# Kernel optimization log

Measured on AMD Instinct MI355X. Metric: run time of the kernel, lower is better.

The kernel has to match this reference:

```python
import math
import jax, jax.numpy as jnp
import numpy as np

B, S, D, H = 4, 2048, 1024, 16
HD = D // H
EPS = 1e-5
NEG = 1e10


def setup_inputs() -> dict:
    key = jax.random.key(0)
    ks = jax.random.split(key, 6)
    std = 0.02
    return {
        "x": jax.random.normal(ks[0], (B, S, D), dtype=jnp.float32),
        "ln1_w": jnp.ones((D,), jnp.float32),
        "ln1_b": jnp.zeros((D,), jnp.float32),
        "W_attn": jax.random.normal(ks[1], (D, 3 * D), jnp.float32) * std,
        "b_attn": jnp.zeros((3 * D,), jnp.float32),
        "W_cproj": jax.random.normal(ks[2], (D, D), jnp.float32) * std,
        "b_cproj": jnp.zeros((D,), jnp.float32),
        "ln2_w": jnp.ones((D,), jnp.float32),
        "ln2_b": jnp.zeros((D,), jnp.float32),
        "W_fc": jax.random.normal(ks[3], (D, 4 * D), jnp.float32) * std,
        "b_fc": jnp.zeros((4 * D,), jnp.float32),
        "W_mproj": jax.random.normal(ks[4], (4 * D, D), jnp.float32) * std,
        "b_mproj": jnp.zeros((D,), jnp.float32),
    }


def _layernorm(x, w, b):
    u = jnp.mean(x, axis=-1, keepdims=True)
    s = jnp.mean((x - u) ** 2, axis=-1, keepdims=True)
    return w * ((x - u) / jnp.sqrt(s + EPS)) + b


def _gelu(x):
    return 0.5 * x * (1 + jnp.tanh(math.sqrt(2 / math.pi) * (x + 0.044715 * x ** 3)))


def _block(x, ln1_w, ln1_b, W_attn, b_attn, W_cproj, b_cproj,
           ln2_w, ln2_b, W_fc, b_fc, W_mproj, b_mproj):
    h = _layernorm(x, ln1_w, ln1_b)
    qkv = h @ W_attn + b_attn                       # [B,S,3D]
    q, k, v = jnp.split(qkv, 3, axis=-1)
    # split heads -> [B,H,S,hd]
    q = q.reshape(B, S, H, HD).transpose(0, 2, 1, 3)
    k = k.reshape(B, S, H, HD).transpose(0, 2, 1, 3)
    v = v.reshape(B, S, H, HD).transpose(0, 2, 1, 3)
    w = jnp.einsum('bhqd,bhkd->bhqk', q, k) / math.sqrt(HD)
    bias = jnp.tril(jnp.ones((S, S), jnp.float32))  # causal mask
    w = w * bias - NEG * (1 - bias)
    w = jax.nn.softmax(w, axis=-1)
    a = jnp.einsum('bhqk,bhkd->bhqd', w, v)
    a = a.transpose(0, 2, 1, 3).reshape(B, S, D)    # merge heads
    a = a @ W_cproj + b_cproj
    x = x + a                                        # residual
    m = _layernorm(x, ln2_w, ln2_b)
    m = _gelu(m @ W_fc + b_fc) @ W_mproj + b_mproj
    return x + m


def reference(x, ln1_w, ln1_b, W_attn, b_attn, W_cproj, b_cproj,
              ln2_w, ln2_b, W_fc, b_fc, W_mproj, b_mproj):
    return _block(x, ln1_w, ln1_b, W_attn, b_attn, W_cproj, b_cproj,
                  ln2_w, ln2_b, W_fc, b_fc, W_mproj, b_mproj)
```

## Files before the change

kernel.cpp:

```cpp
#include <hip/hip_runtime.h>
#include <hip/hip_bf16.h>
#include <math.h>


typedef __attribute__((ext_vector_type(8))) short short8;
typedef __attribute__((ext_vector_type(4))) float floatx4;
typedef __attribute__((ext_vector_type(2))) unsigned int uint2v;

#define MFMA16(a, b, c) __builtin_amdgcn_mfma_f32_16x16x32_bf16((a), (b), (c), 0, 0, 0)

__device__ __forceinline__ short f2bf(float f) {
    union { float f; unsigned u; } a; a.f = f;
    unsigned r = a.u + 0x7fffu + ((a.u >> 16) & 1u);
    return (short)(r >> 16);
}

__device__ __forceinline__ float bf2f(unsigned short u) {
    union { unsigned u; float f; } a; a.u = ((unsigned)u) << 16;
    return a.f;
}

__device__ __forceinline__ float fast_rcp(float x) {
#if defined(__HIP_DEVICE_COMPILE__)
    return __builtin_amdgcn_rcpf(x);
#else
    return 1.0f / x;
#endif
}

__device__ __forceinline__ float gelu_f(float x) {
    const float u = x + 0.044715f * x * x * x;
    const float t = exp2f(2.302118131f * u);
    return x - x * fast_rcp(t + 1.0f);
}

__device__ __forceinline__ void gload_lds16(const short* g, short* l) {
    __builtin_amdgcn_global_load_lds((const __attribute__((address_space(1))) void*)g,
                                     (__attribute__((address_space(3))) void*)l, 16, 0, 0);
}

__global__ void tcast_kernel(const float* __restrict__ W, short* __restrict__ Wt,
                             int K, int N) {
    __shared__ float tile[32][33];
    const int bx = blockIdx.x * 32;
    const int by = blockIdx.y * 32;
    const int tx = threadIdx.x;
    const int ty = threadIdx.y;
#pragma unroll
    for (int i = 0; i < 32; i += 8)
        tile[ty + i][tx] = W[(size_t)(by + ty + i) * N + bx + tx];
    __syncthreads();
#pragma unroll
    for (int i = 0; i < 32; i += 8)
        Wt[(size_t)(bx + ty + i) * K + by + tx] = f2bf(tile[tx][ty + i]);
}

__global__ __launch_bounds__(256) void ln_kernel(const float* __restrict__ x,
                                                 const float* __restrict__ w,
                                                 const float* __restrict__ b,
                                                 short* __restrict__ out) {
    const int row = blockIdx.x;
    const int t = threadIdx.x;
    const float4 v = ((const float4*)(x + (size_t)row * 1024))[t];
    float s = v.x + v.y + v.z + v.w;
    float s2 = v.x * v.x + v.y * v.y + v.z * v.z + v.w * v.w;
#pragma unroll
    for (int d = 32; d >= 1; d >>= 1) {
        s += __shfl_xor(s, d, 64);
        s2 += __shfl_xor(s2, d, 64);
    }
    __shared__ float red[8];
    const int wid = t >> 6, lane = t & 63;
    if (lane == 0) { red[wid * 2] = s; red[wid * 2 + 1] = s2; }
    __syncthreads();
    s = red[0] + red[2] + red[4] + red[6];
    s2 = red[1] + red[3] + red[5] + red[7];
    const float mean = s * (1.f / 1024.f);
    const float var = s2 * (1.f / 1024.f) - mean * mean;
    const float rstd = rsqrtf(var + 1e-5f);
    const float4 wv = ((const float4*)w)[t];
    const float4 bv = ((const float4*)b)[t];
    union { ushort4 u; short sa[4]; } ov;
    ov.sa[0] = f2bf(wv.x * ((v.x - mean) * rstd) + bv.x);
    ov.sa[1] = f2bf(wv.y * ((v.y - mean) * rstd) + bv.y);
    ov.sa[2] = f2bf(wv.z * ((v.z - mean) * rstd) + bv.z);
    ov.sa[3] = f2bf(wv.w * ((v.w - mean) * rstd) + bv.w);
    ((ushort4*)(out + (size_t)row * 1024))[t] = ov.u;
}

__global__ __launch_bounds__(256) void reduce_kernel(
    const unsigned short* __restrict__ p0, const unsigned short* __restrict__ p1,
    const float* __restrict__ bias, const float* __restrict__ res,
    float* __restrict__ out) {
    const int row = blockIdx.x;
    const int t = threadIdx.x;
    const size_t off = (size_t)row * 1024;
    const ushort4 a = ((const ushort4*)(p0 + off))[t];
    const ushort4 c = ((const ushort4*)(p1 + off))[t];
    const float4 r = ((const float4*)(res + off))[t];
    const float4 bv = ((const float4*)bias)[t];
    float4 o;
    o.x = bf2f(a.x) + bf2f(c.x) + bv.x + r.x;
    o.y = bf2f(a.y) + bf2f(c.y) + bv.y + r.y;
    o.z = bf2f(a.z) + bf2f(c.z) + bv.z + r.z;
    o.w = bf2f(a.w) + bf2f(c.w) + bv.w + r.w;
    ((float4*)(out + off))[t] = o;
}

__global__ __launch_bounds__(256) void reduce_ln_kernel(
    const unsigned short* __restrict__ p0, const unsigned short* __restrict__ p1,
    const float* __restrict__ bias, const float* __restrict__ res,
    float* __restrict__ x2out,
    const float* __restrict__ w, const float* __restrict__ b,
    short* __restrict__ hout) {
    const int row = blockIdx.x;
    const int t = threadIdx.x;
    const size_t off = (size_t)row * 1024;
    const ushort4 a = ((const ushort4*)(p0 + off))[t];
    const ushort4 c = ((const ushort4*)(p1 + off))[t];
    const float4 r = ((const float4*)(res + off))[t];
    const float4 bv = ((const float4*)bias)[t];
    float4 v;
    v.x = bf2f(a.x) + bf2f(c.x) + bv.x + r.x;
    v.y = bf2f(a.y) + bf2f(c.y) + bv.y + r.y;
    v.z = bf2f(a.z) + bf2f(c.z) + bv.z + r.z;
    v.w = bf2f(a.w) + bf2f(c.w) + bv.w + r.w;
    ((float4*)(x2out + off))[t] = v;
    float s = v.x + v.y + v.z + v.w;
    float s2 = v.x * v.x + v.y * v.y + v.z * v.z + v.w * v.w;
#pragma unroll
    for (int d = 32; d >= 1; d >>= 1) {
        s += __shfl_xor(s, d, 64);
        s2 += __shfl_xor(s2, d, 64);
    }
    __shared__ float red[8];
    const int wid = t >> 6, lane = t & 63;
    if (lane == 0) { red[wid * 2] = s; red[wid * 2 + 1] = s2; }
    __syncthreads();
    s = red[0] + red[2] + red[4] + red[6];
    s2 = red[1] + red[3] + red[5] + red[7];
    const float mean = s * (1.f / 1024.f);
    const float var = s2 * (1.f / 1024.f) - mean * mean;
    const float rstd = rsqrtf(var + 1e-5f);
    const float4 wv = ((const float4*)w)[t];
    const float4 lb = ((const float4*)b)[t];
    union { ushort4 u; short sa[4]; } ov;
    ov.sa[0] = f2bf(wv.x * ((v.x - mean) * rstd) + lb.x);
    ov.sa[1] = f2bf(wv.y * ((v.y - mean) * rstd) + lb.y);
    ov.sa[2] = f2bf(wv.z * ((v.z - mean) * rstd) + lb.z);
    ov.sa[3] = f2bf(wv.w * ((v.w - mean) * rstd) + lb.w);
    ((ushort4*)(hout + (size_t)row * 1024))[t] = ov.u;
}

template <int EPI>
__global__ __launch_bounds__(256) void gemm_kernel(
    const short* __restrict__ A, const short* __restrict__ Bt,
    const float* __restrict__ bias,
    void* __restrict__ Cout, int M, int N, int Klen, int lda, int ldb) {
    __shared__ __align__(16) short As[128][32];
    __shared__ __align__(16) short Bs[128][32];

    const int tid = threadIdx.x;
    const int wid = tid >> 6;
    const int lane = tid & 63;
    const int quad = lane >> 4;
    const int l16 = lane & 15;
    const int wm = (wid >> 1) * 64;
    const int wn = (wid & 1) * 64;

    const unsigned gx = gridDim.x;
    const unsigned bid2 = blockIdx.x + gx * blockIdx.y;
    const unsigned xcd = bid2 & 7;
    const unsigned loc = bid2 >> 3;
    const unsigned nb = loc % gx;
    const unsigned mhi = loc / gx;
    const int m0 = (int)(mhi * 8 + xcd) * 128;
    const int n0 = (int)nb * 128;
    const int kbase = blockIdx.z * Klen;

    const int lr = lane >> 2;
    const int lc = (lane & 3) * 8;

    floatx4 acc[4][4] = {};

    const short* ga0 = A + (size_t)(m0 + wid * 16 + lr) * lda + kbase + lc;
    const short* ga1 = A + (size_t)(m0 + 64 + wid * 16 + lr) * lda + kbase + lc;
    const short* gb0 = Bt + (size_t)(n0 + wid * 16 + lr) * ldb + kbase + lc;
    const short* gb1 = Bt + (size_t)(n0 + 64 + wid * 16 + lr) * ldb + kbase + lc;
    short* lA0 = &As[wid * 16][0];
    short* lA1 = &As[64 + wid * 16][0];
    short* lB0 = &Bs[wid * 16][0];
    short* lB1 = &Bs[64 + wid * 16][0];

    for (int k0 = 0; k0 < Klen; k0 += 32) {
        gload_lds16(ga0 + k0, lA0);
        gload_lds16(ga1 + k0, lA1);
        gload_lds16(gb0 + k0, lB0);
        gload_lds16(gb1 + k0, lB1);
        __syncthreads();
        short8 af[4], bf[4];
#pragma unroll
        for (int mt = 0; mt < 4; mt++)
            af[mt] = *(const short8*)&As[wm + mt * 16 + l16][quad * 8];
#pragma unroll
        for (int nt = 0; nt < 4; nt++)
            bf[nt] = *(const short8*)&Bs[wn + nt * 16 + l16][quad * 8];
#pragma unroll
        for (int mt = 0; mt < 4; mt++)
#pragma unroll
            for (int nt = 0; nt < 4; nt++)
                acc[mt][nt] = MFMA16(af[mt], bf[nt], acc[mt][nt]);
        __syncthreads();
    }
#pragma unroll
    for (int nt = 0; nt < 4; nt++) {
        const int col = n0 + wn + nt * 16 + l16;
        const float bv = (EPI == 3) ? 0.f : bias[col];
#pragma unroll
        for (int mt = 0; mt < 4; mt++) {
#pragma unroll
            for (int r = 0; r < 4; r++) {
                const int row = m0 + wm + mt * 16 + quad * 4 + r;
                const size_t idx = (size_t)row * N + col;
                float v = acc[mt][nt][r] + bv;
                if constexpr (EPI == 0) {
                    ((short*)Cout)[idx] = f2bf(v);
                } else if constexpr (EPI == 1) {
                    ((short*)Cout)[idx] = f2bf(gelu_f(v));
                } else {
                    ((short*)Cout)[(size_t)blockIdx.z * M * N + idx] = f2bf(v);
                }
            }
        }
    }
}

#define GBAR()  asm volatile("s_barrier" ::: "memory")
#define LGKM0() asm volatile("s_waitcnt lgkmcnt(0)" ::: "memory")
#define STAGE_A(b_, kt_, p_)                                                   \
    do {                                                                       \
        gload_lds16(gA + (size_t)((p_) * 128) * lda + (kt_) * 64,              \
                    lA + (b_) * 16384 + (p_) * 8192);                          \
        gload_lds16(gA + (size_t)((p_) * 128 + 64) * lda + (kt_) * 64,         \
                    lA + (b_) * 16384 + (p_) * 8192 + 4096);                   \
    } while (0)
#define STAGE_B(b_, kt_, p_)                                                   \
    do {                                                                       \
        gload_lds16(gB + (size_t)((p_) * 128) * ldb + (kt_) * 64,              \
                    lB + (b_) * 16384 + (p_) * 8192);                          \
        gload_lds16(gB + (size_t)((p_) * 128 + 64) * ldb + (kt_) * 64,         \
                    lB + (b_) * 16384 + (p_) * 8192 + 4096);                   \
    } while (0)

template <int EPI>
__global__ __launch_bounds__(512, 2) void gemm256_kernel(
    const short* __restrict__ A, const short* __restrict__ Bt,
    const float* __restrict__ bias,
    void* __restrict__ Cout, int M, int N, int Klen, int lda, int ldb) {
    extern __shared__ __align__(16) short lds[];
    short* As = lds;
    short* Bs = lds + 32768;

    const int tid = threadIdx.x;
    const int wid = tid >> 6;
    const int lane = tid & 63;
    const int quad = lane >> 4;
    const int l16 = lane & 15;
    const int l7 = l16 & 7;
    const int warp_m = wid >> 2;
    const int warp_n = wid & 3;

    const unsigned gx = gridDim.x;
    const unsigned bid2 = blockIdx.x + gx * blockIdx.y;
    const unsigned xcd = bid2 & 7;
    const unsigned loc = bid2 >> 3;
    const unsigned nb = loc % gx;
    const unsigned mhi = loc / gx;
    const int m0 = (int)(mhi * 8 + xcd) * 256;
    const int n0 = (int)nb * 256;
    const int kbase = blockIdx.z * Klen;
    const int NT = Klen >> 6;

    const int rsub = tid >> 3;
    const int scol = ((tid & 7) ^ (rsub & 7)) << 3;
    const short* gA = A + (size_t)(m0 + rsub) * lda + kbase + scol;
    const short* gB = Bt + (size_t)(n0 + rsub) * ldb + kbase + scol;
    short* lA = As + wid * 512;
    short* lB = Bs + wid * 512;

    const int sk0 = ((0 | quad) ^ l7) << 3;
    const int sk1 = ((4 | quad) ^ l7) << 3;

    floatx4 acc[8][4] = {};
    short8 afrag[4][2], bA[2][2], bB[2][2];

    STAGE_A(0, 0, 0); STAGE_A(0, 0, 1);
    STAGE_B(0, 0, 0); STAGE_B(0, 0, 1);
    if (NT > 1) {
        STAGE_A(1, 1, 0);
        asm volatile("s_waitcnt vmcnt(2)" ::: "memory");
    } else {
        asm volatile("s_waitcnt vmcnt(0)" ::: "memory");
    }
    GBAR();

    for (int t = 0; t < NT; ++t) {
        const int b = t & 1;
        const int bn = b ^ 1;
        const short* Ab = As + b * 16384 + (warp_m * 128 + l16) * 64;
        const short* Bb = Bs + b * 16384 + (warp_n * 64 + l16) * 64;
#pragma unroll
        for (int mi = 0; mi < 4; mi++) {
            afrag[mi][0] = *(const short8*)(Ab + mi * 1024 + sk0);
            afrag[mi][1] = *(const short8*)(Ab + mi * 1024 + sk1);
        }
#pragma unroll
        for (int ni = 0; ni < 2; ni++) {
            bA[ni][0] = *(const short8*)(Bb + ni * 1024 + sk0);
            bA[ni][1] = *(const short8*)(Bb + ni * 1024 + sk1);
        }
        if (t + 1 < NT) STAGE_A(bn, t + 1, 1);
        GBAR(); LGKM0();
        __builtin_amdgcn_s_setprio(1);
#pragma unroll
        for (int mi = 0; mi < 4; mi++)
#pragma unroll
            for (int ni = 0; ni < 2; ni++) {
                acc[mi][ni] = MFMA16(afrag[mi][0], bA[ni][0], acc[mi][ni]);
                acc[mi][ni] = MFMA16(afrag[mi][1], bA[ni][1], acc[mi][ni]);
            }
        __builtin_amdgcn_s_setprio(0);
        GBAR();
#pragma unroll
        for (int ni = 0; ni < 2; ni++) {
            bB[ni][0] = *(const short8*)(Bb + (2 + ni) * 1024 + sk0);
            bB[ni][1] = *(const short8*)(Bb + (2 + ni) * 1024 + sk1);
        }
        if (t + 1 < NT) STAGE_B(bn, t + 1, 0);
        GBAR(); LGKM0();
        __builtin_amdgcn_s_setprio(1);
#pragma unroll
        for (int mi = 0; mi < 4; mi++)
#pragma unroll
            for (int ni = 0; ni < 2; ni++) {
                acc[mi][2 + ni] = MFMA16(afrag[mi][0], bB[ni][0], acc[mi][2 + ni]);
                acc[mi][2 + ni] = MFMA16(afrag[mi][1], bB[ni][1], acc[mi][2 + ni]);
            }
        __builtin_amdgcn_s_setprio(0);
        GBAR();
#pragma unroll
        for (int mi = 0; mi < 4; mi++) {
            afrag[mi][0] = *(const short8*)(Ab + (4 + mi) * 1024 + sk0);
            afrag[mi][1] = *(const short8*)(Ab + (4 + mi) * 1024 + sk1);
        }
        if (t + 1 < NT) STAGE_B(bn, t + 1, 1);
        GBAR(); LGKM0();
        __builtin_amdgcn_s_setprio(1);
#pragma unroll
        for (int mi = 0; mi < 4; mi++)
#pragma unroll
            for (int ni = 0; ni < 2; ni++) {
                acc[4 + mi][2 + ni] = MFMA16(afrag[mi][0], bB[ni][0], acc[4 + mi][2 + ni]);
                acc[4 + mi][2 + ni] = MFMA16(afrag[mi][1], bB[ni][1], acc[4 + mi][2 + ni]);
            }
        __builtin_amdgcn_s_setprio(0);
        GBAR();
        if (t + 2 < NT) STAGE_A(b, t + 2, 0);
        GBAR();
        __builtin_amdgcn_s_setprio(1);
#pragma unroll
        for (int mi = 0; mi < 4; mi++)
#pragma unroll
            for (int ni = 0; ni < 2; ni++) {
                acc[4 + mi][ni] = MFMA16(afrag[mi][0], bA[ni][0], acc[4 + mi][ni]);
                acc[4 + mi][ni] = MFMA16(afrag[mi][1], bA[ni][1], acc[4 + mi][ni]);
            }
        __builtin_amdgcn_s_setprio(0);
        if (t + 2 < NT) asm volatile("s_waitcnt vmcnt(2)" ::: "memory");
        else            asm volatile("s_waitcnt vmcnt(0)" ::: "memory");
        GBAR();
    }

#pragma unroll
    for (int ni = 0; ni < 4; ni++) {
        const int col = n0 + warp_n * 64 + ni * 16 + l16;
        const float bv = (EPI == 3) ? 0.f : bias[col];
#pragma unroll
        for (int mi = 0; mi < 8; mi++) {
#pragma unroll
            for (int r = 0; r < 4; r++) {
                const int row = m0 + warp_m * 128 + mi * 16 + quad * 4 + r;
                const size_t idx = (size_t)row * N + col;
                float v = acc[mi][ni][r] + bv;
                if constexpr (EPI == 0) {
                    ((short*)Cout)[idx] = f2bf(v);
                } else if constexpr (EPI == 1) {
                    ((short*)Cout)[idx] = f2bf(gelu_f(v));
                } else {
                    ((short*)Cout)[(size_t)blockIdx.z * M * N + idx] = f2bf(v);
                }
            }
        }
    }
}
#undef STAGE_A
#undef STAGE_B
#undef GBAR
#undef LGKM0

__global__ __launch_bounds__(256) void attn_kernel(
    const short* __restrict__ qkv, short* __restrict__ aout,
    short* __restrict__ O0buf, float* __restrict__ m0p, float* __restrict__ l0p,
    float* __restrict__ m1p, float* __restrict__ l1p) {
    __shared__ __align__(16) short smem[9216];
    short* Ks = smem;
    short* Vt = smem + 64 * 72;

    const int tid = threadIdx.x;
    const int wid = tid >> 6;
    const int lane = tid & 63;
    const int quad = lane >> 4;
    const int l16 = lane & 15;

    const int y = blockIdx.y;
    int qt, ktlo, kthi, mode;
    if (y < 8)       { qt = 8 + y;        ktlo = 0;  kthi = 16;             mode = 1; }
    else if (y < 16) { qt = 15 - y;       ktlo = 0;  kthi = (qt + 1) * 2;   mode = 0; }
    else             { qt = 8 + (23 - y); ktlo = 16; kthi = (qt + 1) * 2;   mode = 2; }
    const int q0 = qt * 128;
    const int bh = blockIdx.x;
    const int b = bh >> 4;
    const int h = bh & 15;

    const short* base = qkv + (size_t)b * 2048 * 3072 + h * 64;
    const int qrow_base = q0 + wid * 32;

    short8 qf[2][2];
#pragma unroll
    for (int qt_i = 0; qt_i < 2; qt_i++)
#pragma unroll
        for (int ks = 0; ks < 2; ks++)
            qf[qt_i][ks] = *(const short8*)(base +
                (size_t)(qrow_base + qt_i * 16 + l16) * 3072 + ks * 32 + quad * 8);

    const unsigned vaddr =
        (unsigned)(size_t)(__attribute__((address_space(3))) void*)Vt +
        (unsigned)(quad * 128 + l16 * 8);

    union VF { short8 s; uint2v h2[2]; };
    union PK { short8 s; unsigned u[4]; };

    floatx4 o[4][2] = {};
    float mrow[2] = {-1e30f, -1e30f};
    float lrow[2] = {0.f, 0.f};
    const float SCL = 0.125f * 1.44269504f;

    for (int kt = ktlo; kt < kthi; kt++) {
        const int kt0 = kt * 64;
        {
            const int r = tid >> 2;
            const int dgi = tid & 3;
            const short* krow = base + (size_t)(kt0 + r) * 3072 + 1024 + dgi * 16;
            const short* vrow = base + (size_t)(kt0 + r) * 3072 + 2048 + dgi * 16;
            *(uint4*)&Ks[r * 72 + dgi * 16] = ((const uint4*)krow)[0];
            *(uint4*)&Ks[r * 72 + dgi * 16 + 8] = ((const uint4*)krow)[1];
            short* vdst = Vt + dgi * 1024 + (r >> 2) * 64 + (r & 3) * 16;
            *(uint4*)&vdst[0] = ((const uint4*)vrow)[0];
            *(uint4*)&vdst[8] = ((const uint4*)vrow)[1];
        }
        __syncthreads();
        if (kt0 <= qrow_base + 31) {
            floatx4 st[4][2] = {};
#pragma unroll
            for (int kti = 0; kti < 4; kti++) {
                const short8 kf0 = *(const short8*)&Ks[(kti * 16 + l16) * 72 + quad * 8];
                const short8 kf1 = *(const short8*)&Ks[(kti * 16 + l16) * 72 + 32 + quad * 8];
#pragma unroll
                for (int qt_i = 0; qt_i < 2; qt_i++) {
                    st[kti][qt_i] = MFMA16(kf0, qf[qt_i][0], st[kti][qt_i]);
                    st[kti][qt_i] = MFMA16(kf1, qf[qt_i][1], st[kti][qt_i]);
                }
            }
            VF vf[2][4];
#define TRRD(dst, offs) \
    asm volatile("ds_read_b64_tr_b16 %0, %1 offset:" offs : "=v"(dst) : "v"(vaddr))
            TRRD(vf[0][0].h2[0], "0");    TRRD(vf[0][0].h2[1], "512");
            TRRD(vf[0][1].h2[0], "2048"); TRRD(vf[0][1].h2[1], "2560");
            TRRD(vf[0][2].h2[0], "4096"); TRRD(vf[0][2].h2[1], "4608");
            TRRD(vf[0][3].h2[0], "6144"); TRRD(vf[0][3].h2[1], "6656");
            TRRD(vf[1][0].h2[0], "1024"); TRRD(vf[1][0].h2[1], "1536");
            TRRD(vf[1][1].h2[0], "3072"); TRRD(vf[1][1].h2[1], "3584");
            TRRD(vf[1][2].h2[0], "5120"); TRRD(vf[1][2].h2[1], "5632");
            TRRD(vf[1][3].h2[0], "7168"); TRRD(vf[1][3].h2[1], "7680");
#undef TRRD
            const bool needmask = (kt0 + 63) > qrow_base;
            PK pk[2][2];
#pragma unroll
            for (int qt_i = 0; qt_i < 2; qt_i++) {
                const int q = qrow_base + qt_i * 16 + l16;
                if (needmask) {
#pragma unroll
                    for (int kti = 0; kti < 4; kti++)
#pragma unroll
                        for (int r = 0; r < 4; r++)
                            if ((kt0 + kti * 16 + quad * 4 + r) > q) st[kti][qt_i][r] = -1e30f;
                }
                float mx = -1e30f;
#pragma unroll
                for (int kti = 0; kti < 4; kti++)
#pragma unroll
                    for (int r = 0; r < 4; r++) mx = fmaxf(mx, st[kti][qt_i][r]);
                mx = fmaxf(mx, __shfl_xor(mx, 16, 64));
                mx = fmaxf(mx, __shfl_xor(mx, 32, 64));
                const float mnew = fmaxf(mrow[qt_i], mx);
                const float alpha = exp2f((mrow[qt_i] - mnew) * SCL);
                mrow[qt_i] = mnew;
                const float nm = -mnew * SCL;
                float ps = 0.f;
#pragma unroll
                for (int kti = 0; kti < 4; kti++)
#pragma unroll
                    for (int r = 0; r < 4; r++) {
                        const float p = exp2f(fmaf(st[kti][qt_i][r], SCL, nm));
                        st[kti][qt_i][r] = p;
                        ps += p;
                    }
                ps += __shfl_xor(ps, 16, 64);
                ps += __shfl_xor(ps, 32, 64);
                lrow[qt_i] = lrow[qt_i] * alpha + ps;
#pragma unroll
                for (int dt = 0; dt < 4; dt++) o[dt][qt_i] *= alpha;
#define CVTPK(dst, lo, hi) \
    asm("v_cvt_pk_bf16_f32 %0, %1, %2" : "=v"(dst) : "v"(lo), "v"(hi))
                CVTPK(pk[0][qt_i].u[0], st[0][qt_i][0], st[0][qt_i][1]);
                CVTPK(pk[0][qt_i].u[1], st[0][qt_i][2], st[0][qt_i][3]);
                CVTPK(pk[0][qt_i].u[2], st[1][qt_i][0], st[1][qt_i][1]);
                CVTPK(pk[0][qt_i].u[3], st[1][qt_i][2], st[1][qt_i][3]);
                CVTPK(pk[1][qt_i].u[0], st[2][qt_i][0], st[2][qt_i][1]);
                CVTPK(pk[1][qt_i].u[1], st[2][qt_i][2], st[2][qt_i][3]);
                CVTPK(pk[1][qt_i].u[2], st[3][qt_i][0], st[3][qt_i][1]);
                CVTPK(pk[1][qt_i].u[3], st[3][qt_i][2], st[3][qt_i][3]);
#undef CVTPK
            }
            asm volatile("s_waitcnt lgkmcnt(0)" ::: "memory");
            __builtin_amdgcn_sched_barrier(0);
#pragma unroll
            for (int c = 0; c < 2; c++)
#pragma unroll
                for (int dt = 0; dt < 4; dt++) {
                    o[dt][0] = MFMA16(vf[c][dt].s, pk[c][0].s, o[dt][0]);
                    o[dt][1] = MFMA16(vf[c][dt].s, pk[c][1].s, o[dt][1]);
                }
        }
        __syncthreads();
    }
    const int slot = (qt - 8) * 64 + bh;
    short* Ow = smem + wid * (32 * 72);
    const float rl0 = (mode == 0) ? fast_rcp(lrow[0]) : 1.0f;
    const float rl1 = (mode == 0) ? fast_rcp(lrow[1]) : 1.0f;
#pragma unroll
    for (int dt = 0; dt < 4; dt++)
#pragma unroll
        for (int r = 0; r < 4; r++) {
            Ow[(l16) * 72 + dt * 16 + quad * 4 + r] = f2bf(o[dt][0][r] * rl0);
            Ow[(16 + l16) * 72 + dt * 16 + quad * 4 + r] = f2bf(o[dt][1][r] * rl1);
        }
    if (mode != 0 && quad == 0) {
        const int qi0 = slot * 128 + (qrow_base - q0) + l16;
        if (mode == 1) {
            m0p[qi0] = mrow[0]; l0p[qi0] = lrow[0];
            m0p[qi0 + 16] = mrow[1]; l0p[qi0 + 16] = lrow[1];
        } else {
            m1p[qi0] = mrow[0]; l1p[qi0] = lrow[0];
            m1p[qi0 + 16] = mrow[1]; l1p[qi0 + 16] = lrow[1];
        }
    }
    __asm__ volatile("s_waitcnt lgkmcnt(0)" ::: "memory");
    {
        const int ql = lane >> 1;
        const int h2 = lane & 1;
        short* orow;
        if (mode == 1)
            orow = O0buf + (size_t)slot * 8192 + (size_t)(wid * 32 + ql) * 64 + h2 * 32;
        else
            orow = aout + (size_t)(b * 2048 + q0 + wid * 32 + ql) * 1024 + h * 64 + h2 * 32;
#pragma unroll
        for (int s = 0; s < 4; s++)
            *(uint4*)(orow + s * 8) = *(const uint4*)&Ow[ql * 72 + h2 * 32 + s * 8];
    }
}

__global__ __launch_bounds__(256) void attn_combine_kernel(
    const short* __restrict__ O0buf, short* __restrict__ aout,
    const float* __restrict__ m0p, const float* __restrict__ l0p,
    const float* __restrict__ m1p, const float* __restrict__ l1p) {
    const int slot = blockIdx.x;
    const int qt = 8 + (slot >> 6);
    const int bh = slot & 63;
    const int b = bh >> 4;
    const int h = bh & 15;
    const int t = threadIdx.x;
    const float SCL = 0.125f * 1.44269504f;
#pragma unroll
    for (int rep = 0; rep < 2; rep++) {
        const int ql = rep * 64 + (t >> 2);
        const int dg = (t & 3) * 16;
        const int qi = slot * 128 + ql;
        const float m0 = m0p[qi], l0 = l0p[qi], m1 = m1p[qi], l1 = l1p[qi];
        const float mm = fmaxf(m0, m1);
        const float w0 = exp2f((m0 - mm) * SCL);
        const float w1 = exp2f((m1 - mm) * SCL);
        const float rl = fast_rcp(fmaf(l0, w0, l1 * w1));
        const float f0 = w0 * rl, f1 = w1 * rl;
        const short* p0 = O0buf + (size_t)slot * 8192 + (size_t)ql * 64 + dg;
        short* pout = aout + (size_t)(b * 2048 + qt * 128 + ql) * 1024 + h * 64 + dg;
        union { uint4 v; unsigned short u[8]; } a0, a1, ov;
#pragma unroll
        for (int half = 0; half < 2; half++) {
            a0.v = ((const uint4*)p0)[half];
            a1.v = ((const uint4*)pout)[half];
#pragma unroll
            for (int j = 0; j < 8; j++)
                ov.u[j] = (unsigned short)f2bf(bf2f(a0.u[j]) * f0 + bf2f(a1.u[j]) * f1);
            ((uint4*)pout)[half] = ov.v;
        }
    }
}

extern "C" void kernel_launch(void* const* d_in, const int* in_sizes, int n_in,
                              void* d_out, int out_size, void* d_ws, size_t ws_size,
                              hipStream_t stream) {
    const float* x       = (const float*)d_in[0];
    const float* ln1_w   = (const float*)d_in[1];
    const float* ln1_b   = (const float*)d_in[2];
    const float* W_attn  = (const float*)d_in[3];
    const float* b_attn  = (const float*)d_in[4];
    const float* W_cproj = (const float*)d_in[5];
    const float* b_cproj = (const float*)d_in[6];
    const float* ln2_w   = (const float*)d_in[7];
    const float* ln2_b   = (const float*)d_in[8];
    const float* W_fc    = (const float*)d_in[9];
    const float* b_fc    = (const float*)d_in[10];
    const float* W_mproj = (const float*)d_in[11];
    const float* b_mproj = (const float*)d_in[12];

    char* ws = (char*)d_ws;
    short* W1t  = (short*)(ws + 0);
    short* W2t  = (short*)(ws + 6291456);
    short* W3t  = (short*)(ws + 8388608);
    short* W4t  = (short*)(ws + 16777216);
    short* h    = (short*)(ws + 25165824);
    short* aout = (short*)(ws + 41943040);
    short* big  = (short*)(ws + 58720256);
    short* O0buf = h;
    float* m0p = (float*)(ws + 25165824 + 8388608);
    float* l0p = (float*)(ws + 25165824 + 8388608 + 262144);
    float* m1p = (float*)(ws + 25165824 + 8388608 + 524288);
    float* l1p = (float*)(ws + 25165824 + 8388608 + 786432);
    short* pbuf = h;
    float* x2   = (float*)d_out;
    float* out  = (float*)d_out;

    dim3 tb(32, 8);
    hipLaunchKernelGGL(tcast_kernel, dim3(96, 32), tb, 0, stream, W_attn, W1t, 1024, 3072);
    hipLaunchKernelGGL(tcast_kernel, dim3(32, 32), tb, 0, stream, W_cproj, W2t, 1024, 1024);
    hipLaunchKernelGGL(tcast_kernel, dim3(128, 32), tb, 0, stream, W_fc, W3t, 1024, 4096);
    hipLaunchKernelGGL(tcast_kernel, dim3(32, 128), tb, 0, stream, W_mproj, W4t, 4096, 1024);

    hipLaunchKernelGGL(ln_kernel, dim3(8192), dim3(256), 0, stream, x, ln1_w, ln1_b, h);

    hipLaunchKernelGGL((gemm256_kernel<0>), dim3(12, 32, 1), dim3(512), 131072, stream,
                       h, W1t, b_attn, (void*)big,
                       8192, 3072, 1024, 1024, 1024);

    hipLaunchKernelGGL(attn_kernel, dim3(64, 24), dim3(256), 0, stream,
                       big, aout, O0buf, m0p, l0p, m1p, l1p);
    hipLaunchKernelGGL(attn_combine_kernel, dim3(512), dim3(256), 0, stream,
                       O0buf, aout, m0p, l0p, m1p, l1p);

    hipLaunchKernelGGL((gemm_kernel<3>), dim3(8, 64, 2), dim3(256), 0, stream,
                       aout, W2t, (const float*)nullptr, (void*)big,
                       8192, 1024, 512, 1024, 1024);
    hipLaunchKernelGGL(reduce_ln_kernel, dim3(8192), dim3(256), 0, stream,
                       (const unsigned short*)big,
                       (const unsigned short*)(big + (size_t)8192 * 1024),
                       b_cproj, x, x2, ln2_w, ln2_b, h);

    hipLaunchKernelGGL((gemm256_kernel<1>), dim3(16, 32, 1), dim3(512), 131072, stream,
                       h, W3t, b_fc, (void*)big,
                       8192, 4096, 1024, 1024, 1024);

    hipLaunchKernelGGL((gemm256_kernel<3>), dim3(4, 32, 2), dim3(512), 131072, stream,
                       big, W4t, (const float*)nullptr, (void*)pbuf,
                       8192, 1024, 2048, 4096, 4096);
    hipLaunchKernelGGL(reduce_kernel, dim3(8192), dim3(256), 0, stream,
                       (const unsigned short*)pbuf,
                       (const unsigned short*)(pbuf + (size_t)8192 * 1024),
                       b_mproj, x2, out);
}
```

Baseline: 533.2 us.

## Register-prefetch next K/V tile in attention and use 256-tile GEMM for c_proj

The attention loop now loads the next K and V tile from global memory into registers while the current tile is being computed, then writes those registers to shared memory at the top of the next iteration. This hides global load latency behind the MFMA work. The V remap to the transposed layout is recomputed per lane so that each lane stores contiguous 16-byte chunks. Separately, the attention output projection switches from the 128-tile split-K GEMM to the 256-tile GEMM kernel. This changes the grid from 1024 to 256 blocks, which risks lower occupancy and a tail effect.

```diff
diff --git a/kernel.cpp b/kernel.cpp
--- a/kernel.cpp
+++ b/kernel.cpp
@@ -443,6 +443,14 @@
             qf[qt_i][ks] = *(const short8*)(base +
                 (size_t)(qrow_base + qt_i * 16 + l16) * 3072 + ks * 32 + quad * 8);
 
+    const int kr_ = tid >> 2;
+    const int kcg = (tid & 3) * 16;
+    const short* ksrc = base + 1024 + kcg;
+    short* kdst = &Ks[kr_ * 72 + kcg];
+    const int vrA = ((lane >> 3) << 2) | ((lane >> 1) & 3);
+    const short* vsrc = base + 2048 + wid * 16 + (lane & 1) * 8;
+    short* vdst = Vt + wid * 1024 + lane * 8;
+
     const unsigned vaddr =
         (unsigned)(size_t)(__attribute__((address_space(3))) void*)Vt +
         (unsigned)(quad * 128 + l16 * 8);
@@ -455,19 +463,24 @@
     float lrow[2] = {0.f, 0.f};
     const float SCL = 0.125f * 1.44269504f;
 
+    uint4 krg0, krg1, vrg0, vrg1;
+#define LOADREG(kt0_)                                                          \
+    do {                                                                       \
+        const short* kp = ksrc + (size_t)((kt0_) + kr_) * 3072;                \
+        krg0 = ((const uint4*)kp)[0];                                          \
+        krg1 = ((const uint4*)kp)[1];                                          \
+        vrg0 = *(const uint4*)(vsrc + (size_t)((kt0_) + vrA) * 3072);          \
+        vrg1 = *(const uint4*)(vsrc + (size_t)((kt0_) + vrA + 32) * 3072);     \
+    } while (0)
+
+    LOADREG(ktlo * 64);
     for (int kt = ktlo; kt < kthi; kt++) {
         const int kt0 = kt * 64;
-        {
-            const int r = tid >> 2;
-            const int dgi = tid & 3;
-            const short* krow = base + (size_t)(kt0 + r) * 3072 + 1024 + dgi * 16;
-            const short* vrow = base + (size_t)(kt0 + r) * 3072 + 2048 + dgi * 16;
-            *(uint4*)&Ks[r * 72 + dgi * 16] = ((const uint4*)krow)[0];
-            *(uint4*)&Ks[r * 72 + dgi * 16 + 8] = ((const uint4*)krow)[1];
-            short* vdst = Vt + dgi * 1024 + (r >> 2) * 64 + (r & 3) * 16;
-            *(uint4*)&vdst[0] = ((const uint4*)vrow)[0];
-            *(uint4*)&vdst[8] = ((const uint4*)vrow)[1];
-        }
+        *(uint4*)kdst = krg0;
+        *(uint4*)(kdst + 8) = krg1;
+        *(uint4*)vdst = vrg0;
+        *(uint4*)(vdst + 512) = vrg1;
+        if (kt + 1 < kthi) LOADREG((kt + 1) * 64);
         __syncthreads();
         if (kt0 <= qrow_base + 31) {
             floatx4 st[4][2] = {};
@@ -554,6 +567,7 @@
         }
         __syncthreads();
     }
+#undef LOADREG
     const int slot = (qt - 8) * 64 + bh;
     short* Ow = smem + wid * (32 * 72);
     const float rl0 = (mode == 0) ? fast_rcp(lrow[0]) : 1.0f;
@@ -678,7 +692,7 @@
     hipLaunchKernelGGL(attn_combine_kernel, dim3(512), dim3(256), 0, stream,
                        O0buf, aout, m0p, l0p, m1p, l1p);
 
-    hipLaunchKernelGGL((gemm_kernel<3>), dim3(8, 64, 2), dim3(256), 0, stream,
+    hipLaunchKernelGGL((gemm256_kernel<3>), dim3(4, 32, 2), dim3(512), 131072, stream,
                        aout, W2t, (const float*)nullptr, (void*)big,
                        8192, 1024, 512, 1024, 1024);
     hipLaunchKernelGGL(reduce_ln_kernel, dim3(8192), dim3(256), 0, stream,
```

After: 524.0 us. No clear change (-1.7%).
